# Optimization experiments

Measured on AMD Instinct MI355X. Metric: run time of the kernel, lower is better.

## Reference

```python
import jax, jax.numpy as jnp
import numpy as np

B, S, D_IN, E, H = 4, 2048, 768, 768, 12
HD = E // H                      # 64
WIN_PCT = 10                     # window_size init arg (percent of valid length)
MAX_LEN = 2048
MIN_WIN = 2
PAD = -1e9
TEMP = 1.0


def setup_inputs() -> dict:
    key = jax.random.key(0)
    k1, k2, k3 = jax.random.split(key, 3)
    return {
        "x": jax.random.normal(k1, (B, S, D_IN), dtype=jnp.float32),
        "src_key_padding_mask": jnp.zeros((B, S), dtype=jnp.int32),   # 0 = valid token
        "matrix_mask": jnp.zeros((B, S, S), dtype=jnp.float32),       # additive mask, 0 or PAD
        "qkv_w": jax.random.normal(k2, (3 * E, D_IN), dtype=jnp.float32) * 0.02,
        "qkv_b": jnp.zeros((3 * E,), dtype=jnp.float32),
        "o_w": jax.random.normal(k3, (E, E), dtype=jnp.float32) * 0.02,
        "o_b": jnp.zeros((E,), dtype=jnp.float32),
    }


def _sliding_window_mask(src_key_padding_mask, matrix_mask):
    # per-sample window size = ceil(valid_len * WIN_PCT / 100), clamped to >= MIN_WIN
    lens = (src_key_padding_mask == 0).sum(axis=1)                    # [B]
    clipped = jnp.minimum(lens, MAX_LEN).astype(jnp.float32)
    wsz = jnp.maximum(jnp.ceil(clipped * WIN_PCT / 100.0), MIN_WIN)   # [B] float ok for compare
    idx = jnp.arange(S)
    dist = jnp.abs(idx[None, :, None] - idx[None, None, :])           # [1,S,S]
    window_mask = dist > wsz[:, None, None]                           # [B,S,S] bool
    merged = window_mask | (matrix_mask == PAD)
    return jnp.where(merged, PAD, matrix_mask)                        # [B,S,S]


def reference(x, src_key_padding_mask, matrix_mask, qkv_w, qkv_b, o_w, o_b):
    mask = _sliding_window_mask(src_key_padding_mask, matrix_mask)    # [B,S,S]
    qkv = x @ qkv_w.T + qkv_b                                         # [B,S,3E]
    # torch: reshape(B,S,H,3*HD) then chunk along last dim
    qkv = qkv.reshape(B, S, H, 3 * HD).transpose(0, 2, 1, 3)          # [B,H,S,3*HD]
    q, k, v = jnp.split(qkv, 3, axis=-1)                              # each [B,H,S,HD]
    scale = 1.0 / np.sqrt(HD)
    logits = jnp.einsum("bhqd,bhkd->bhqk", q, k) * scale + mask[:, None]
    attn = jax.nn.softmax(logits / TEMP, axis=-1)                     # [B,H,S,S]
    values = jnp.einsum("bhqk,bhkd->bhqd", attn, v)                   # [B,H,S,HD]
    attn_mean = attn.mean(axis=1)                                     # [B,S,S]
    values = values.transpose(0, 2, 1, 3).reshape(B, S, E)            # [B,S,E]
    o = values @ o_w.T + o_b
    return (o, attn_mean)
```

## Files before the change

### kernel.cpp

```cpp
#include <hip/hip_runtime.h>

#define SEQ 2048
#define NB 4
#define DIN 768
#define EDIM 768
#define NH 12
#define QKVN 2304
#define QKW 1536
#define SCALE 0.125f
#define PADV -1e9f
#define INV12 (0.0833333333f)
#define PSW 520

typedef unsigned short ushort_t;
typedef __attribute__((ext_vector_type(8))) short bf16x8;
typedef __attribute__((ext_vector_type(4))) float f32x4;

__device__ __forceinline__ float bf2f(ushort_t u) {
    union { unsigned int i; float f; } v; v.i = ((unsigned int)u) << 16; return v.f;
}
__device__ __forceinline__ ushort_t f2bf(float f) {
    union { float f; unsigned int i; } v; v.f = f;
    unsigned int r = (v.i + 0x7fffu + ((v.i >> 16) & 1u)) >> 16;
    return (ushort_t)r;
}
__device__ __forceinline__ void gl_lds16(const ushort_t* g, ushort_t* l) {
    __builtin_amdgcn_global_load_lds(
        (const __attribute__((address_space(1))) unsigned int*)(g),
        (__attribute__((address_space(3))) unsigned int*)(l),
        16, 0, 0);
}

__global__ void wsz_kernel(const int* __restrict__ mask, int* __restrict__ wszp) {
    int b = blockIdx.x;
    __shared__ int cnt;
    if (threadIdx.x == 0) cnt = 0;
    __syncthreads();
    int local = 0;
    for (int s = threadIdx.x; s < SEQ; s += blockDim.x)
        local += (mask[b * SEQ + s] == 0) ? 1 : 0;
    for (int o = 32; o; o >>= 1) local += __shfl_down(local, o, 64);
    if ((threadIdx.x & 63) == 0) atomicAdd(&cnt, local);
    __syncthreads();
    if (threadIdx.x == 0) {
        int len = cnt; if (len > 2048) len = 2048;
        float w = ceilf(((float)len * 10.0f) / 100.0f);
        int wsz = (int)w;
        if (wsz < 2) wsz = 2;
        wszp[b] = wsz;
    }
}

__global__ void cvt_kernel(const float* __restrict__ in, ushort_t* __restrict__ out, int n4) {
    int i = blockIdx.x * blockDim.x + threadIdx.x;
    if (i < n4) {
        float4 f = ((const float4*)in)[i];
        ushort4 u;
        u.x = f2bf(f.x); u.y = f2bf(f.y); u.z = f2bf(f.z); u.w = f2bf(f.w);
        ((ushort4*)out)[i] = u;
    }
}

__global__ void flag_kernel(const float* __restrict__ mmask, const int* __restrict__ wszp,
                            int* __restrict__ flags) {
    const int b = blockIdx.z, i16 = blockIdx.y;
    const int wsz = wszp[b];
    const int i0 = i16 * 16;
    const int jt0 = max(0, i0 - wsz) >> 6;
    const int jt1 = min(SEQ - 1, i0 + 15 + wsz) >> 6;
    const int jt = jt0 + blockIdx.x;
    if (jt > jt1) return;
    int any = 0;
    for (int e = threadIdx.x; e < 1024; e += 256) {
        int row = e >> 6, col = e & 63;
        float v = mmask[((size_t)b * SEQ + i0 + row) * SEQ + jt * 64 + col];
        any |= (v != 0.f);
    }
    if (any) flags[(b * 128 + i16) * 32 + jt] = 1;
}

template<int MODE>
__global__ __launch_bounds__(256) void mfma_gemm128(
    const ushort_t* __restrict__ A, const ushort_t* __restrict__ Bw,
    const float* __restrict__ bias, float* __restrict__ outf,
    ushort_t* __restrict__ qk, ushort_t* __restrict__ vt, int N, int K)
{
    __shared__ __align__(16) ushort_t Al[128 * 64];
    __shared__ __align__(16) ushort_t Bl[128 * 64];
    const int tid  = threadIdx.x;
    const int w    = tid >> 6;
    const int l    = tid & 63;
    const int quad = l >> 4;
    const int lr   = l & 15;
    const int mw   = (w >> 1) * 64;
    const int nw   = (w & 1) * 64;
    const int bm   = blockIdx.y * 128;
    const int bn   = blockIdx.x * 128;
    const int srow = l >> 3;
    const int sg   = (l & 7) ^ srow;

    f32x4 acc[4][4];
    #pragma unroll
    for (int i = 0; i < 4; ++i)
        #pragma unroll
        for (int j = 0; j < 4; ++j)
            #pragma unroll
            for (int r = 0; r < 4; ++r) acc[i][j][r] = 0.f;

    const ushort_t* ga = A  + (size_t)(bm + w * 32 + srow) * K + sg * 8;
    const ushort_t* gb = Bw + (size_t)(bn + w * 32 + srow) * K + sg * 8;
    ushort_t* la = &Al[(w * 32) * 64];
    ushort_t* lb = &Bl[(w * 32) * 64];

    for (int k0 = 0; k0 < K; k0 += 64) {
        __syncthreads();
        #pragma unroll
        for (int i = 0; i < 4; ++i)
            gl_lds16(ga + (size_t)(i * 8) * K + k0, la + i * 8 * 64);
        #pragma unroll
        for (int i = 0; i < 4; ++i)
            gl_lds16(gb + (size_t)(i * 8) * K + k0, lb + i * 8 * 64);
        __syncthreads();
        #pragma unroll
        for (int s = 0; s < 2; ++s) {
            bf16x8 af[4], bf[4];
            #pragma unroll
            for (int t = 0; t < 4; ++t)
                af[t] = *(const bf16x8*)&Al[(mw + t * 16 + lr) * 64 + (((4 * s + quad) ^ (lr & 7)) * 8)];
            #pragma unroll
            for (int t = 0; t < 4; ++t)
                bf[t] = *(const bf16x8*)&Bl[(nw + t * 16 + lr) * 64 + (((4 * s + quad) ^ (lr & 7)) * 8)];
            #pragma unroll
            for (int mt = 0; mt < 4; ++mt)
                #pragma unroll
                for (int nt = 0; nt < 4; ++nt)
                    acc[mt][nt] = __builtin_amdgcn_mfma_f32_16x16x32_bf16(af[mt], bf[nt], acc[mt][nt], 0, 0, 0);
        }
    }

    #pragma unroll
    for (int nt = 0; nt < 4; ++nt) {
        const int gn = bn + nw + nt * 16 + lr;
        const float bv = bias[gn];
        const int hh  = gn / 192;
        const int rem = gn - hh * 192;
        #pragma unroll
        for (int mt = 0; mt < 4; ++mt) {
            const int gm0 = bm + mw + mt * 16 + quad * 4;
            if (MODE == 0) {
                #pragma unroll
                for (int r = 0; r < 4; ++r)
                    outf[(size_t)(gm0 + r) * N + gn] = acc[mt][nt][r] + bv;
            } else if (rem < 128) {
                #pragma unroll
                for (int r = 0; r < 4; ++r)
                    qk[(size_t)(gm0 + r) * QKW + hh * 128 + rem] = f2bf(acc[mt][nt][r] + bv);
            } else {
                const int bb  = gm0 >> 11;
                const int tok = gm0 & (SEQ - 1);
                ushort4 st;
                st.x = f2bf(acc[mt][nt][0] + bv);
                st.y = f2bf(acc[mt][nt][1] + bv);
                st.z = f2bf(acc[mt][nt][2] + bv);
                st.w = f2bf(acc[mt][nt][3] + bv);
                *(ushort4*)&vt[((size_t)(bb * NH + hh) * 64 + (rem - 128)) * SEQ + tok] = st;
            }
        }
    }
}

__global__ __launch_bounds__(256) void attn_kernel(
    const ushort_t* __restrict__ qk,
    const ushort_t* __restrict__ vt,
    const float* __restrict__ mmask,
    const int* __restrict__ wszp,
    const int* __restrict__ flags,
    ushort_t* __restrict__ values,
    float* __restrict__ attn_out)
{
    __shared__ __align__(16) ushort_t Ps[16 * PSW];
    __shared__ float lsump[4][16];
    const int tid  = threadIdx.x;
    const int w    = tid >> 6;
    const int lane = tid & 63;
    const int quad = lane >> 4;
    const int lr   = lane & 15;

    const int lin  = blockIdx.x;
    const int s    = lin & 1;
    const int b    = (lin >> 1) & 3;
    const int i16  = (lin >> 3) + 64 * s;
    const int iq0  = i16 * 16;

    const int wsz  = wszp[b];
    const int jlo  = max(0, iq0 - wsz);
    const int jhi  = min(SEQ - 1, iq0 + 15 + wsz);
    const int jt0  = jlo >> 6;
    const int nch  = (jhi >> 6) - jt0 + 1;
    const int jbase = jt0 << 6;
    const int span  = nch << 6;
    const int fbase = (b * 128 + i16) * 32;

    const int arow = tid & 15;
    const int acg  = tid >> 4;
    float acc[32];
    #pragma unroll
    for (int k = 0; k < 32; ++k) acc[k] = 0.f;

    const ushort_t* kbase = qk + (size_t)b * SEQ * QKW + 64;
    const ushort_t* vhead = vt + (size_t)b * NH * 64 * SEQ;

    for (int h = 0; h < NH; ++h) {
        const int hq = h * 128;
        const ushort_t* qbase = qk + (size_t)(b * SEQ + iq0 + lr) * QKW + hq;
        const bf16x8 qf0 = *(const bf16x8*)(qbase + quad * 8);
        const bf16x8 qf1 = *(const bf16x8*)(qbase + 32 + quad * 8);

        float ls[4] = {0.f, 0.f, 0.f, 0.f};
        #pragma unroll
        for (int cc = 0; cc < 2; ++cc) {
            const int ci = w + cc * 4;
            if (ci < nch) {
                const int jc = jbase + ci * 64;
                f32x4 s4[4];
                #pragma unroll
                for (int t = 0; t < 4; ++t) {
                    const ushort_t* kr = kbase + (size_t)(jc + t * 16 + lr) * QKW + hq;
                    bf16x8 kf0 = *(const bf16x8*)(kr + quad * 8);
                    bf16x8 kf1 = *(const bf16x8*)(kr + 32 + quad * 8);
                    #pragma unroll
                    for (int r = 0; r < 4; ++r) s4[t][r] = 0.f;
                    s4[t] = __builtin_amdgcn_mfma_f32_16x16x32_bf16(qf0, kf0, s4[t], 0, 0, 0);
                    s4[t] = __builtin_amdgcn_mfma_f32_16x16x32_bf16(qf1, kf1, s4[t], 0, 0, 0);
                }
                const int anym = flags[fbase + jt0 + ci];
                #pragma unroll
                for (int t = 0; t < 4; ++t) {
                    const int gj = jc + t * 16 + lr;
                    #pragma unroll
                    for (int r = 0; r < 4; ++r) {
                        const int gi = iq0 + quad * 4 + r;
                        float mm = 0.f;
                        if (anym) mm = mmask[((size_t)b * SEQ + gi) * SEQ + gj];
                        const int dist = gi > gj ? gi - gj : gj - gi;
                        const float p = (dist > wsz) ? 0.f : __expf(fmaf(s4[t][r], SCALE, mm));
                        ls[r] += p;
                        Ps[(quad * 4 + r) * PSW + (ci * 64 + t * 16 + lr)] = f2bf(p);
                    }
                }
            }
        }
        #pragma unroll
        for (int r = 0; r < 4; ++r) {
            #pragma unroll
            for (int m = 8; m; m >>= 1) ls[r] += __shfl_xor(ls[r], m, 16);
        }
        if (lr == 0) {
            #pragma unroll
            for (int r = 0; r < 4; ++r) lsump[w][quad * 4 + r] = ls[r];
        }
        __syncthreads();

        if (acg * 32 < span) {
            const float lrow = lsump[0][arow] + lsump[1][arow] + lsump[2][arow] + lsump[3][arow];
            const float sc = INV12 / lrow;
            const ushort_t* prow = &Ps[arow * PSW + acg * 32];
            #pragma unroll
            for (int k = 0; k < 8; ++k) {
                ushort4 u = *(const ushort4*)(prow + k * 4);
                acc[k * 4 + 0] = fmaf(bf2f(u.x), sc, acc[k * 4 + 0]);
                acc[k * 4 + 1] = fmaf(bf2f(u.y), sc, acc[k * 4 + 1]);
                acc[k * 4 + 2] = fmaf(bf2f(u.z), sc, acc[k * 4 + 2]);
                acc[k * 4 + 3] = fmaf(bf2f(u.w), sc, acc[k * 4 + 3]);
            }
        }

        {
            f32x4 oacc;
            #pragma unroll
            for (int r = 0; r < 4; ++r) oacc[r] = 0.f;
            const ushort_t* vrow = vhead + (size_t)(h * 64 + w * 16 + lr) * SEQ + jbase;
            for (int ci = 0; ci < nch; ++ci) {
                const int tok0 = ci * 64;
                #pragma unroll
                for (int s2 = 0; s2 < 2; ++s2) {
                    bf16x8 pa = *(const bf16x8*)&Ps[lr * PSW + tok0 + s2 * 32 + quad * 8];
                    bf16x8 vf = *(const bf16x8*)(vrow + tok0 + s2 * 32 + quad * 8);
                    oacc = __builtin_amdgcn_mfma_f32_16x16x32_bf16(pa, vf, oacc, 0, 0, 0);
                }
            }
            float4 lq = *(const float4*)&lsump[0][quad * 4];
            float4 l1 = *(const float4*)&lsump[1][quad * 4];
            float4 l2 = *(const float4*)&lsump[2][quad * 4];
            float4 l3 = *(const float4*)&lsump[3][quad * 4];
            float lr4[4] = { lq.x + l1.x + l2.x + l3.x, lq.y + l1.y + l2.y + l3.y,
                             lq.z + l1.z + l2.z + l3.z, lq.w + l1.w + l2.w + l3.w };
            #pragma unroll
            for (int r = 0; r < 4; ++r) {
                const int row = iq0 + quad * 4 + r;
                values[(size_t)(b * SEQ + row) * EDIM + h * 64 + w * 16 + lr] =
                    f2bf(oacc[r] / lr4[r]);
            }
        }
        __syncthreads();
    }

    if (acg * 32 < span) {
        float* dst = attn_out + ((size_t)b * SEQ + iq0 + arow) * SEQ + jbase + acg * 32;
        #pragma unroll
        for (int k = 0; k < 8; ++k) {
            float4 v = { acc[k * 4 + 0], acc[k * 4 + 1], acc[k * 4 + 2], acc[k * 4 + 3] };
            *(float4*)(dst + k * 4) = v;
        }
    }
    {
        const int c4lo = jbase >> 2;
        const int c4hi = (jbase + span) >> 2;
        const float4 z = {0.f, 0.f, 0.f, 0.f};
        for (int f = tid; f < 16 * 512; f += 256) {
            const int i  = f >> 9;
            const int c4 = f & 511;
            if (c4 < c4lo || c4 >= c4hi)
                *(float4*)(attn_out + ((size_t)b * SEQ + iq0 + i) * SEQ + c4 * 4) = z;
        }
    }
}

extern "C" void kernel_launch(void* const* d_in, const int* in_sizes, int n_in,
                              void* d_out, int out_size, void* d_ws, size_t ws_size,
                              hipStream_t stream) {
    const float* x      = (const float*)d_in[0];
    const int*   pad    = (const int*)d_in[1];
    const float* mmask  = (const float*)d_in[2];
    const float* qkv_w  = (const float*)d_in[3];
    const float* qkv_b  = (const float*)d_in[4];
    const float* o_w    = (const float*)d_in[5];
    const float* o_b    = (const float*)d_in[6];

    float* out_o    = (float*)d_out;
    float* out_attn = out_o + (size_t)NB * SEQ * EDIM;

    ushort_t* qk     = (ushort_t*)d_ws;
    ushort_t* vt     = qk + (size_t)NB * SEQ * QKW;
    ushort_t* xb     = vt + (size_t)NB * NH * 64 * SEQ;
    ushort_t* values = xb;
    ushort_t* wqkvb  = xb + (size_t)NB * SEQ * DIN;
    ushort_t* wob    = wqkvb + (size_t)QKVN * DIN;
    int*      wszp   = (int*)(wob + (size_t)EDIM * EDIM);
    int*      flags  = wszp + 4;

    hipMemsetAsync(flags, 0, (size_t)NB * 128 * 32 * sizeof(int), stream);

    wsz_kernel<<<NB, 256, 0, stream>>>(pad, wszp);
    flag_kernel<<<dim3(8, 128, NB), 256, 0, stream>>>(mmask, wszp, flags);

    const int nx = NB * SEQ * DIN / 4, nw1 = QKVN * DIN / 4, nw2 = EDIM * EDIM / 4;
    cvt_kernel<<<(nx  + 255) / 256, 256, 0, stream>>>(x,     xb,    nx);
    cvt_kernel<<<(nw1 + 255) / 256, 256, 0, stream>>>(qkv_w, wqkvb, nw1);
    cvt_kernel<<<(nw2 + 255) / 256, 256, 0, stream>>>(o_w,   wob,   nw2);

    mfma_gemm128<1><<<dim3(QKVN / 128, (NB * SEQ) / 128), 256, 0, stream>>>(
        xb, wqkvb, qkv_b, nullptr, qk, vt, QKVN, DIN);

    attn_kernel<<<512, 256, 0, stream>>>(
        qk, vt, mmask, wszp, flags, values, out_attn);

    mfma_gemm128<0><<<dim3(EDIM / 128, (NB * SEQ) / 128), 256, 0, stream>>>(
        values, wob, o_b, out_o, nullptr, nullptr, EDIM, EDIM);
}
```

Before: 372.2 us.

## Process two heads concurrently per attention block with 512 threads

Doubles the attention block to 512 threads (8 waves) so two heads are handled at once, each half of the block using its own P tile and row-sum buffer. The head loop runs six iterations instead of twelve, and the head-mean accumulation combines both heads' probabilities per step, which halves the per-thread accumulator registers. The aim is more parallel work per block and fewer barrier-separated iterations on a grid of only 512 blocks, at the cost of double the shared memory and more register pressure per block.

```diff
diff --git a/kernel.cpp b/kernel.cpp
--- a/kernel.cpp
+++ b/kernel.cpp
@@ -169,7 +169,7 @@
     }
 }
 
-__global__ __launch_bounds__(256) void attn_kernel(
+__global__ __launch_bounds__(512) void attn_kernel(
     const ushort_t* __restrict__ qk,
     const ushort_t* __restrict__ vt,
     const float* __restrict__ mmask,
@@ -178,10 +178,12 @@
     ushort_t* __restrict__ values,
     float* __restrict__ attn_out)
 {
-    __shared__ __align__(16) ushort_t Ps[16 * PSW];
-    __shared__ float lsump[4][16];
+    __shared__ __align__(16) ushort_t Ps[2][16 * PSW];
+    __shared__ float lsump[2][4][16];
     const int tid  = threadIdx.x;
     const int w    = tid >> 6;
+    const int hg   = w >> 2;
+    const int ww   = w & 3;
     const int lane = tid & 63;
     const int quad = lane >> 4;
     const int lr   = lane & 15;
@@ -203,14 +205,15 @@
 
     const int arow = tid & 15;
     const int acg  = tid >> 4;
-    float acc[32];
+    float acc[16];
     #pragma unroll
-    for (int k = 0; k < 32; ++k) acc[k] = 0.f;
+    for (int k = 0; k < 16; ++k) acc[k] = 0.f;
 
     const ushort_t* kbase = qk + (size_t)b * SEQ * QKW + 64;
     const ushort_t* vhead = vt + (size_t)b * NH * 64 * SEQ;
 
-    for (int h = 0; h < NH; ++h) {
+    for (int hp = 0; hp < NH / 2; ++hp) {
+        const int h  = hp * 2 + hg;
         const int hq = h * 128;
         const ushort_t* qbase = qk + (size_t)(b * SEQ + iq0 + lr) * QKW + hq;
         const bf16x8 qf0 = *(const bf16x8*)(qbase + quad * 8);
@@ -219,7 +222,7 @@
         float ls[4] = {0.f, 0.f, 0.f, 0.f};
         #pragma unroll
         for (int cc = 0; cc < 2; ++cc) {
-            const int ci = w + cc * 4;
+            const int ci = ww + cc * 4;
             if (ci < nch) {
                 const int jc = jbase + ci * 64;
                 f32x4 s4[4];
@@ -245,7 +248,7 @@
                         const int dist = gi > gj ? gi - gj : gj - gi;
                         const float p = (dist > wsz) ? 0.f : __expf(fmaf(s4[t][r], SCALE, mm));
                         ls[r] += p;
-                        Ps[(quad * 4 + r) * PSW + (ci * 64 + t * 16 + lr)] = f2bf(p);
+                        Ps[hg][(quad * 4 + r) * PSW + (ci * 64 + t * 16 + lr)] = f2bf(p);
                     }
                 }
             }
@@ -257,21 +260,25 @@
         }
         if (lr == 0) {
             #pragma unroll
-            for (int r = 0; r < 4; ++r) lsump[w][quad * 4 + r] = ls[r];
+            for (int r = 0; r < 4; ++r) lsump[hg][ww][quad * 4 + r] = ls[r];
         }
         __syncthreads();
 
-        if (acg * 32 < span) {
-            const float lrow = lsump[0][arow] + lsump[1][arow] + lsump[2][arow] + lsump[3][arow];
-            const float sc = INV12 / lrow;
-            const ushort_t* prow = &Ps[arow * PSW + acg * 32];
-            #pragma unroll
-            for (int k = 0; k < 8; ++k) {
-                ushort4 u = *(const ushort4*)(prow + k * 4);
-                acc[k * 4 + 0] = fmaf(bf2f(u.x), sc, acc[k * 4 + 0]);
-                acc[k * 4 + 1] = fmaf(bf2f(u.y), sc, acc[k * 4 + 1]);
-                acc[k * 4 + 2] = fmaf(bf2f(u.z), sc, acc[k * 4 + 2]);
-                acc[k * 4 + 3] = fmaf(bf2f(u.w), sc, acc[k * 4 + 3]);
+        if (acg * 16 < span) {
+            const float l0 = lsump[0][0][arow] + lsump[0][1][arow] + lsump[0][2][arow] + lsump[0][3][arow];
+            const float l1 = lsump[1][0][arow] + lsump[1][1][arow] + lsump[1][2][arow] + lsump[1][3][arow];
+            const float sc0 = INV12 / l0;
+            const float sc1 = INV12 / l1;
+            const ushort_t* p0 = &Ps[0][arow * PSW + acg * 16];
+            const ushort_t* p1 = &Ps[1][arow * PSW + acg * 16];
+            #pragma unroll
+            for (int k = 0; k < 4; ++k) {
+                ushort4 u0 = *(const ushort4*)(p0 + k * 4);
+                ushort4 u1 = *(const ushort4*)(p1 + k * 4);
+                acc[k * 4 + 0] = fmaf(bf2f(u0.x), sc0, fmaf(bf2f(u1.x), sc1, acc[k * 4 + 0]));
+                acc[k * 4 + 1] = fmaf(bf2f(u0.y), sc0, fmaf(bf2f(u1.y), sc1, acc[k * 4 + 1]));
+                acc[k * 4 + 2] = fmaf(bf2f(u0.z), sc0, fmaf(bf2f(u1.z), sc1, acc[k * 4 + 2]));
+                acc[k * 4 + 3] = fmaf(bf2f(u0.w), sc0, fmaf(bf2f(u1.w), sc1, acc[k * 4 + 3]));
             }
         }
 
@@ -279,36 +286,35 @@
             f32x4 oacc;
             #pragma unroll
             for (int r = 0; r < 4; ++r) oacc[r] = 0.f;
-            const ushort_t* vrow = vhead + (size_t)(h * 64 + w * 16 + lr) * SEQ + jbase;
+            const ushort_t* vrow = vhead + (size_t)(hq / 2 + ww * 16 + lr) * SEQ + jbase;
             for (int ci = 0; ci < nch; ++ci) {
                 const int tok0 = ci * 64;
                 #pragma unroll
                 for (int s2 = 0; s2 < 2; ++s2) {
-                    bf16x8 pa = *(const bf16x8*)&Ps[lr * PSW + tok0 + s2 * 32 + quad * 8];
+                    bf16x8 pa = *(const bf16x8*)&Ps[hg][lr * PSW + tok0 + s2 * 32 + quad * 8];
                     bf16x8 vf = *(const bf16x8*)(vrow + tok0 + s2 * 32 + quad * 8);
                     oacc = __builtin_amdgcn_mfma_f32_16x16x32_bf16(pa, vf, oacc, 0, 0, 0);
                 }
             }
-            float4 lq = *(const float4*)&lsump[0][quad * 4];
-            float4 l1 = *(const float4*)&lsump[1][quad * 4];
-            float4 l2 = *(const float4*)&lsump[2][quad * 4];
-            float4 l3 = *(const float4*)&lsump[3][quad * 4];
-            float lr4[4] = { lq.x + l1.x + l2.x + l3.x, lq.y + l1.y + l2.y + l3.y,
-                             lq.z + l1.z + l2.z + l3.z, lq.w + l1.w + l2.w + l3.w };
+            float lr4[4];
+            #pragma unroll
+            for (int r = 0; r < 4; ++r)
+                lr4[r] = lsump[hg][0][quad * 4 + r] + lsump[hg][1][quad * 4 + r] +
+                         lsump[hg][2][quad * 4 + r] + lsump[hg][3][quad * 4 + r];
             #pragma unroll
             for (int r = 0; r < 4; ++r) {
                 const int row = iq0 + quad * 4 + r;
-                values[(size_t)(b * SEQ + row) * EDIM + h * 64 + w * 16 + lr] =
+                values[(size_t)(b * SEQ + row) * EDIM + h * 64 + ww * 16 + lr] =
                     f2bf(oacc[r] / lr4[r]);
             }
         }
         __syncthreads();
     }
 
-    if (acg * 32 < span) {
-        float* dst = attn_out + ((size_t)b * SEQ + iq0 + arow) * SEQ + jbase + acg * 32;
-        #pragma unroll
-        for (int k = 0; k < 8; ++k) {
+    if (acg * 16 < span) {
+        float* dst = attn_out + ((size_t)b * SEQ + iq0 + arow) * SEQ + jbase + acg * 16;
+        #pragma unroll
+        for (int k = 0; k < 4; ++k) {
             float4 v = { acc[k * 4 + 0], acc[k * 4 + 1], acc[k * 4 + 2], acc[k * 4 + 3] };
             *(float4*)(dst + k * 4) = v;
         }
@@ -317,7 +323,7 @@
         const int c4lo = jbase >> 2;
         const int c4hi = (jbase + span) >> 2;
         const float4 z = {0.f, 0.f, 0.f, 0.f};
-        for (int f = tid; f < 16 * 512; f += 256) {
+        for (int f = tid; f < 16 * 512; f += 512) {
             const int i  = f >> 9;
             const int c4 = f & 511;
             if (c4 < c4lo || c4 >= c4hi)
@@ -362,7 +368,7 @@
     mfma_gemm128<1><<<dim3(QKVN / 128, (NB * SEQ) / 128), 256, 0, stream>>>(
         xb, wqkvb, qkv_b, nullptr, qk, vt, QKVN, DIN);
 
-    attn_kernel<<<512, 256, 0, stream>>>(
+    attn_kernel<<<512, 512, 0, stream>>>(
         qk, vt, mmask, wszp, flags, values, out_attn);
 
     mfma_gemm128<0><<<dim3(EDIM / 128, (NB * SEQ) / 128), 256, 0, stream>>>(
```

Result: faster. 345.1 us (-7.3%).
